# Performance work log

Hardware: AMD Instinct MI355X
Metric: run time of the kernel (lower is better)

Reference implementation:

```python
import jax, jax.numpy as jnp
import numpy as np

# dims
B, S, H = 2, 256, 1024          # batch, global seq, global hidden
BH, NH = 384, 8                  # byte_hidden, num heads
HD = BH // NH                    # head dim = 48
P = 4                            # num_global_proj (seed byte positions)
S_C = 12                         # byte decode steps (= target.shape[2])
L = 4                            # num_byte_decoder_layers
V = 258                          # byte vocab (256 bytes + pad 256 + eos 257)
T = P + S_C
EOS = 257
SCALE = 1.0 / np.sqrt(HD)


def setup_inputs() -> dict:
    key = jax.random.key(0)
    ks = jax.random.split(key, 12)
    w = lambda k, shp: jax.random.normal(k, shp, jnp.float32) * 0.02
    return {
        "x": jax.random.normal(ks[0], (B, S, H), jnp.float32),
        "target": jax.random.randint(ks[1], (B, S, S_C), 0, V),
        "Wproj": w(ks[2], (H, P * BH)),
        "attn_norm": jnp.ones((L, BH), jnp.float32),
        "Wq": w(ks[3], (L, BH, BH)),
        "Wk": w(ks[4], (L, BH, BH)),
        "Wv": w(ks[5], (L, BH, BH)),
        "Wo": w(ks[6], (L, BH, BH)),
        "ffn_norm": jnp.ones((L, BH), jnp.float32),
        "W1": w(ks[7], (L, BH, 4 * BH)),
        "W2": w(ks[8], (L, 4 * BH, BH)),
        "Wlm": w(ks[9], (BH, V)),
    }


def _rms(x, g):
    return x * jax.lax.rsqrt(jnp.mean(x * x, -1, keepdims=True) + 1e-5) * g


def _block(x, kc, vc, pos, an, Wq, Wk, Wv, Wo, fn, W1, W2, causal):
    # x: [N, Lq, BH]; kc/vc: [N, T, NH, HD] KV caches; pos: static write offset
    N, Lq, _ = x.shape
    h = _rms(x, an)
    q = (h @ Wq).reshape(N, Lq, NH, HD)
    k = (h @ Wk).reshape(N, Lq, NH, HD)
    v = (h @ Wv).reshape(N, Lq, NH, HD)
    kc = jax.lax.dynamic_update_slice(kc, k, (0, pos, 0, 0))
    vc = jax.lax.dynamic_update_slice(vc, v, (0, pos, 0, 0))
    nk = pos + Lq
    sc = jnp.einsum('nqhd,nkhd->nhqk', q, kc[:, :nk]) * SCALE
    if causal:
        mask = jnp.arange(nk)[None, :] <= (pos + jnp.arange(Lq))[:, None]
        sc = jnp.where(mask[None, None], sc, jnp.float32(-1e30))
    p = jax.nn.softmax(sc, axis=-1)
    o = jnp.einsum('nhqk,nkhd->nqhd', p, vc[:, :nk]).reshape(N, Lq, BH)
    x = x + o @ Wo
    x = x + jax.nn.gelu(_rms(x, fn) @ W1, approximate=False) @ W2
    return x, kc, vc


def _forward(x, Wproj, attn_norm, Wq, Wk, Wv, Wo, ffn_norm, W1, W2, Wlm):
    N = B * S
    x0 = (x.reshape(N, H) @ Wproj).reshape(N, P, BH)
    x_out = jnp.zeros((N, T, BH), x0.dtype).at[:, :P].set(x0)
    kc = [jnp.zeros((N, T, NH, HD), x0.dtype) for _ in range(L)]
    vc = [jnp.zeros((N, T, NH, HD), x0.dtype) for _ in range(L)]
    finished = jnp.zeros((N,), bool)
    for i in range(S_C):
        if i == 0:
            pos, xi, causal = 0, x_out[:, :P], True          # prefill seed bytes
        else:
            pos, xi, causal = P + i - 1, x_out[:, P + i - 1:P + i], False  # decode 1 token
        for l in range(L):
            xi, kc[l], vc[l] = _block(xi, kc[l], vc[l], pos,
                                      attn_norm[l], Wq[l], Wk[l], Wv[l], Wo[l],
                                      ffn_norm[l], W1[l], W2[l], causal)
        gen = xi[:, -1]                                       # [N, BH]
        unf = ~finished
        # scatter only unfinished streams back (finished stay zero, as in torch)
        x_out = x_out.at[:, P + i].set(jnp.where(unf[:, None], gen, jnp.float32(0.0)))
        finished = finished | (unf & (jnp.argmax(gen, -1) == EOS))
    return x_out.reshape(B, S, T, BH)[:, :, P:, :] @ Wlm      # [B,S,S_C,V]


def reference(x, target, Wproj, attn_norm, Wq, Wk, Wv, Wo, ffn_norm, W1, W2, Wlm):
    del target  # only sets S_c (static here)
    return _forward(x, Wproj, attn_norm, Wq, Wk, Wv, Wo, ffn_norm, W1, W2, Wlm)
```

## Files before the change

### kernel.cpp

```cpp
#include <hip/hip_runtime.h>
#include <hip/hip_bf16.h>


constexpr int H_IN  = 1024;
constexpr int BH    = 384;
constexpr int NH    = 8;
constexpr int HD    = 48;
constexpr int PP    = 4;
constexpr int S_CNT = 12;
constexpr int NL    = 4;
constexpr int NV    = 258;
constexpr int TT    = 16;
constexpr int NSEQ  = 512;
constexpr int EOS_I = 257;
constexpr int NTH   = 768;
constexpr float RSCALE = 0.14433756729740646f;

typedef _Float16 h2 __attribute__((ext_vector_type(2)));
typedef _Float16 h8 __attribute__((ext_vector_type(8)));

union W16 { h8 v8; h2 h[4]; _Float16 e[8]; };

template<int N> struct IC { static constexpr int value = N; };

__device__ __forceinline__ float fdot2(h2 a, h2 b, float c) {
#if __has_builtin(__builtin_amdgcn_fdot2)
  return __builtin_amdgcn_fdot2(a, b, c, false);
#else
  return c + (float)a.x * (float)b.x + (float)a.y * (float)b.y;
#endif
}

__global__ __launch_bounds__(256)
void pack8_kernel(const float* __restrict__ src, const float* __restrict__ g,
                  h8* __restrict__ dst, int C) {
  int c  = blockIdx.x * 256 + threadIdx.x;
  int j8 = blockIdx.y;
  if (c < C) {
    h8 v;
    #pragma unroll
    for (int r = 0; r < 8; r++) {
      int row = 8 * j8 + r;
      float s = g ? g[row] : 1.0f;
      v[r] = (_Float16)(src[(size_t)row * C + c] * s);
    }
    dst[(size_t)j8 * C + c] = v;
  }
}

__global__ __launch_bounds__(NTH)
void decoder_kernel(const float* __restrict__ x,
                    const h8* __restrict__ Wproj8,
                    const h8* __restrict__ Wq8,
                    const h8* __restrict__ Wk8,
                    const h8* __restrict__ Wv8,
                    const h8* __restrict__ Wo8,
                    const h8* __restrict__ W18,
                    const h8* __restrict__ W28,
                    const h8* __restrict__ Wlm8,
                    float* __restrict__ out,
                    _Float16* __restrict__ kbuf,
                    _Float16* __restrict__ vbuf)
{
  __shared__ float xs[2][4][BH];
  __shared__ __align__(16) _Float16 xh[2][4][BH];
  __shared__ __align__(16) _Float16 qh[2][4][BH];
  __shared__ __align__(16) _Float16 oh[2][4][BH];
  __shared__ __align__(16) _Float16 k_cur[2][4][BH];
  __shared__ __align__(16) _Float16 v_cur[2][4][BH];
  __shared__ float sc[2][NH][4][TT];
  __shared__ __align__(16) union Scr {
    float qkvp[3][2][4][BH];
    float wop[2][4][BH];
    struct { __align__(16) _Float16 f1h[2][4][4*BH];
             float w2p[2][4][BH]; } ffn;
    __align__(16) _Float16 xin[2][H_IN];
  } scr;
  __shared__ float redsq[2][4][6];
  __shared__ float redv[12];
  __shared__ int   redi[12];
  __shared__ int   fin[2];

  const int tid = threadIdx.x;
  const int kg  = tid / BH;
  const int col = tid - kg * BH;
  const int sq  = kg;
  const int wid = tid >> 6;
  const int w6  = wid % 6;
  const int seq0 = blockIdx.x * 2;

  if (tid < 2) fin[tid] = 0;

  for (int s = 0; s < 2; s++) {
    const size_t base = (size_t)(seq0 + s) * H_IN;
    for (int j = tid; j < H_IN; j += NTH) scr.xin[s][j] = (_Float16)x[base + j];
  }
  __syncthreads();
  {
    float acc[2][2] = {};
    for (int j8 = 0; j8 < H_IN / 8; j8 += 4) {
      W16 w0[4], w1[4];
      #pragma unroll
      for (int u = 0; u < 4; u++) {
        w0[u].v8 = Wproj8[(size_t)(j8 + u) * (PP * BH) + tid];
        w1[u].v8 = Wproj8[(size_t)(j8 + u) * (PP * BH) + tid + NTH];
      }
      #pragma unroll
      for (int u = 0; u < 4; u++)
        #pragma unroll
        for (int s = 0; s < 2; s++) {
          W16 hv; hv.v8 = *(const h8*)&scr.xin[s][(j8 + u) * 8];
          #pragma unroll
          for (int r = 0; r < 4; r++) {
            acc[s][0] = fdot2(hv.h[r], w0[u].h[r], acc[s][0]);
            acc[s][1] = fdot2(hv.h[r], w1[u].h[r], acc[s][1]);
          }
        }
    }
    const int m0 = tid / BH, cc = tid - m0 * BH;
    #pragma unroll
    for (int s = 0; s < 2; s++) {
      xs[s][m0][cc]     = acc[s][0];  xh[s][m0][cc]     = (_Float16)acc[s][0];
      xs[s][m0 + 2][cc] = acc[s][1];  xh[s][m0 + 2][cc] = (_Float16)acc[s][1];
      float r0 = acc[s][0] * acc[s][0], r1 = acc[s][1] * acc[s][1];
      #pragma unroll
      for (int off = 32; off; off >>= 1) {
        r0 += __shfl_down(r0, off, 64); r1 += __shfl_down(r1, off, 64);
      }
      if ((tid & 63) == 0) { redsq[s][m0][w6] = r0; redsq[s][m0 + 2][w6] = r1; }
    }
  }
  __syncthreads();

  auto layers = [&](auto ntc, int pos, bool causal) {
    constexpr int NT = decltype(ntc)::value;
    const int nk = pos + NT;
    for (int l = 0; l < NL; l++) {
      {
        const size_t wb = ((size_t)l * 48 + kg * 24) * BH + col;
        float aq[2][NT] = {}, ak[2][NT] = {}, av[2][NT] = {};
        for (int j8 = 0; j8 < 24; j8 += 4) {
          W16 wq[4], wk[4], wv[4];
          #pragma unroll
          for (int u = 0; u < 4; u++) {
            wq[u].v8 = Wq8[wb + (size_t)(j8 + u) * BH];
            wk[u].v8 = Wk8[wb + (size_t)(j8 + u) * BH];
            wv[u].v8 = Wv8[wb + (size_t)(j8 + u) * BH];
          }
          #pragma unroll
          for (int u = 0; u < 4; u++)
            #pragma unroll
            for (int s = 0; s < 2; s++)
              #pragma unroll
              for (int tok = 0; tok < NT; tok++) {
                W16 hv; hv.v8 = *(const h8*)&xh[s][tok][(kg * 24 + j8 + u) * 8];
                #pragma unroll
                for (int r = 0; r < 4; r++) {
                  aq[s][tok] = fdot2(hv.h[r], wq[u].h[r], aq[s][tok]);
                  ak[s][tok] = fdot2(hv.h[r], wk[u].h[r], ak[s][tok]);
                  av[s][tok] = fdot2(hv.h[r], wv[u].h[r], av[s][tok]);
                }
              }
        }
        {
          const int so = kg ^ 1;
          #pragma unroll
          for (int tok = 0; tok < NT; tok++) {
            scr.qkvp[0][so][tok][col] = aq[so][tok];
            scr.qkvp[1][so][tok][col] = ak[so][tok];
            scr.qkvp[2][so][tok][col] = av[so][tok];
          }
        }
        __syncthreads();
        {
          const int s = kg;
          const size_t cb = (((size_t)(seq0 + s) * NL + l) * TT + pos) * BH + col;
          #pragma unroll
          for (int tok = 0; tok < NT; tok++) {
            float ss = redsq[s][tok][0] + redsq[s][tok][1] + redsq[s][tok][2] +
                       redsq[s][tok][3] + redsq[s][tok][4] + redsq[s][tok][5];
            float sca = rsqrtf(ss * (1.0f / BH) + 1e-5f);
            float kv_ = (ak[s][tok] + scr.qkvp[1][s][tok][col]) * sca;
            float vv_ = (av[s][tok] + scr.qkvp[2][s][tok][col]) * sca;
            qh[s][tok][col] = (_Float16)((aq[s][tok] + scr.qkvp[0][s][tok][col]) * sca * RSCALE);
            k_cur[s][tok][col] = (_Float16)kv_;
            v_cur[s][tok][col] = (_Float16)vv_;
            kbuf[cb + (size_t)tok * BH] = (_Float16)kv_;
            vbuf[cb + (size_t)tok * BH] = (_Float16)vv_;
          }
        }
        __syncthreads();
      }
      if constexpr (NT == 1) {
        if (tid < 2 * NH * TT) {
          const int s = tid >> 7, r = tid & 127, h = r >> 4, j = r & 15;
          float d = -1e30f;
          if (j < nk) {
            const h8* kp8 = (j == pos)
                ? (const h8*)&k_cur[s][0][h * HD]
                : (const h8*)(kbuf + (((size_t)(seq0 + s) * NL + l) * TT + j) * BH + h * HD);
            d = 0.f;
            #pragma unroll
            for (int c6 = 0; c6 < 6; c6++) {
              W16 kk, qq;
              kk.v8 = kp8[c6];
              qq.v8 = *(const h8*)&qh[s][0][h * HD + c6 * 8];
              #pragma unroll
              for (int rr = 0; rr < 4; rr++) d = fdot2(qq.h[rr], kk.h[rr], d);
            }
          }
          float m = d;
          #pragma unroll
          for (int off = 8; off; off >>= 1) m = fmaxf(m, __shfl_xor(m, off, 16));
          float e = expf(d - m);
          float den = e;
          #pragma unroll
          for (int off = 8; off; off >>= 1) den += __shfl_xor(den, off, 16);
          sc[s][h][0][j] = e * (1.0f / den);
        }
        __syncthreads();
      } else {
        {
          const int nu = 2 * NH * NT * nk;
          if (tid < nu) {
            int s = tid / (NH * NT * nk), r = tid % (NH * NT * nk);
            int h = r / (NT * nk); int r2 = r % (NT * nk);
            int qi = r2 / nk, j = r2 % nk;
            float d;
            if (causal && j > pos + qi) d = -1e30f;
            else {
              d = 0.f;
              #pragma unroll
              for (int c6 = 0; c6 < 6; c6++) {
                W16 kk, qq;
                kk.v8 = *(const h8*)&k_cur[s][j][h * HD + c6 * 8];
                qq.v8 = *(const h8*)&qh[s][qi][h * HD + c6 * 8];
                #pragma unroll
                for (int rr = 0; rr < 4; rr++) d = fdot2(qq.h[rr], kk.h[rr], d);
              }
            }
            sc[s][h][qi][j] = d;
          }
        }
        __syncthreads();
        {
          const int nr = 2 * NH * NT;
          if (tid < nr) {
            int s = tid / (NH * NT), r = tid % (NH * NT);
            int h = r / NT, qi = r % NT;
            float m = -3.0e38f;
            for (int j = 0; j < nk; j++) m = fmaxf(m, sc[s][h][qi][j]);
            float den = 0.f;
            for (int j = 0; j < nk; j++) {
              float e = expf(sc[s][h][qi][j] - m);
              sc[s][h][qi][j] = e; den += e;
            }
            float inv = 1.0f / den;
            for (int j = 0; j < nk; j++) sc[s][h][qi][j] *= inv;
          }
        }
        __syncthreads();
      }
      {
        const size_t vb = (((size_t)(seq0 + sq) * NL + l) * TT) * BH + col;
        const int h = col / HD;
        #pragma unroll
        for (int tok = 0; tok < NT; tok++) {
          float acc = 0.f;
          if constexpr (NT == 1) {
            int j = 0;
            for (; j + 4 <= pos; j += 4) {
              float v0 = (float)vbuf[vb + (size_t)(j + 0) * BH];
              float v1 = (float)vbuf[vb + (size_t)(j + 1) * BH];
              float v2 = (float)vbuf[vb + (size_t)(j + 2) * BH];
              float v3 = (float)vbuf[vb + (size_t)(j + 3) * BH];
              acc += sc[sq][h][0][j] * v0 + sc[sq][h][0][j + 1] * v1 +
                     sc[sq][h][0][j + 2] * v2 + sc[sq][h][0][j + 3] * v3;
            }
            for (; j < pos; j++)
              acc += sc[sq][h][0][j] * (float)vbuf[vb + (size_t)j * BH];
            acc += sc[sq][h][0][pos] * (float)v_cur[sq][0][col];
          } else {
            #pragma unroll
            for (int j = 0; j < 4; j++)
              acc += sc[sq][h][tok][j] * (float)v_cur[sq][j][col];
          }
          oh[sq][tok][col] = (_Float16)acc;
        }
      }
      __syncthreads();
      {
        const size_t wb = ((size_t)l * 48 + kg * 24) * BH + col;
        float ao[2][NT] = {};
        for (int j8 = 0; j8 < 24; j8 += 8) {
          W16 w[8];
          #pragma unroll
          for (int u = 0; u < 8; u++) w[u].v8 = Wo8[wb + (size_t)(j8 + u) * BH];
          #pragma unroll
          for (int u = 0; u < 8; u++)
            #pragma unroll
            for (int s = 0; s < 2; s++)
              #pragma unroll
              for (int tok = 0; tok < NT; tok++) {
                W16 hv; hv.v8 = *(const h8*)&oh[s][tok][(kg * 24 + j8 + u) * 8];
                #pragma unroll
                for (int r = 0; r < 4; r++)
                  ao[s][tok] = fdot2(hv.h[r], w[u].h[r], ao[s][tok]);
              }
        }
        {
          const int so = kg ^ 1;
          #pragma unroll
          for (int tok = 0; tok < NT; tok++) scr.wop[so][tok][col] = ao[so][tok];
        }
        __syncthreads();
        {
          const int s = kg;
          #pragma unroll
          for (int tok = 0; tok < NT; tok++) {
            float xn = xs[s][tok][col] + ao[s][tok] + scr.wop[s][tok][col];
            xs[s][tok][col] = xn; xh[s][tok][col] = (_Float16)xn;
            float r = xn * xn;
            #pragma unroll
            for (int off = 32; off; off >>= 1) r += __shfl_down(r, off, 64);
            if ((tid & 63) == 0) redsq[s][tok][w6] = r;
          }
        }
        __syncthreads();
      }
      {
        float a1[2][NT][2] = {};
        for (int j8 = 0; j8 < 48; j8 += 4) {
          W16 w0[4], w1[4];
          #pragma unroll
          for (int u = 0; u < 4; u++) {
            w0[u].v8 = W18[((size_t)(l * 48 + j8 + u)) * (4 * BH) + tid];
            w1[u].v8 = W18[((size_t)(l * 48 + j8 + u)) * (4 * BH) + tid + NTH];
          }
          #pragma unroll
          for (int u = 0; u < 4; u++)
            #pragma unroll
            for (int s = 0; s < 2; s++)
              #pragma unroll
              for (int t = 0; t < NT; t++) {
                W16 hv; hv.v8 = *(const h8*)&xh[s][t][(j8 + u) * 8];
                #pragma unroll
                for (int r = 0; r < 4; r++) {
                  a1[s][t][0] = fdot2(hv.h[r], w0[u].h[r], a1[s][t][0]);
                  a1[s][t][1] = fdot2(hv.h[r], w1[u].h[r], a1[s][t][1]);
                }
              }
        }
        #pragma unroll
        for (int s = 0; s < 2; s++)
          #pragma unroll
          for (int t = 0; t < NT; t++) {
            float ss = redsq[s][t][0] + redsq[s][t][1] + redsq[s][t][2] +
                       redsq[s][t][3] + redsq[s][t][4] + redsq[s][t][5];
            float sca = rsqrtf(ss * (1.0f / BH) + 1e-5f);
            float z0 = a1[s][t][0] * sca, z1 = a1[s][t][1] * sca;
            scr.ffn.f1h[s][t][tid]       = (_Float16)(0.5f * z0 * (1.0f + erff(z0 * 0.7071067811865476f)));
            scr.ffn.f1h[s][t][tid + NTH] = (_Float16)(0.5f * z1 * (1.0f + erff(z1 * 0.7071067811865476f)));
          }
        __syncthreads();
        {
          float a2[2][NT] = {};
          for (int j8 = 0; j8 < 96; j8 += 8) {
            W16 w[8];
            #pragma unroll
            for (int u = 0; u < 8; u++)
              w[u].v8 = W28[((size_t)(l * 192 + kg * 96 + j8 + u)) * BH + col];
            #pragma unroll
            for (int u = 0; u < 8; u++)
              #pragma unroll
              for (int s = 0; s < 2; s++)
                #pragma unroll
                for (int t = 0; t < NT; t++) {
                  W16 fv; fv.v8 = *(const h8*)&scr.ffn.f1h[s][t][(kg * 96 + j8 + u) * 8];
                  #pragma unroll
                  for (int r = 0; r < 4; r++)
                    a2[s][t] = fdot2(fv.h[r], w[u].h[r], a2[s][t]);
                }
          }
          {
            const int so = kg ^ 1;
            #pragma unroll
            for (int t = 0; t < NT; t++) scr.ffn.w2p[so][t][col] = a2[so][t];
          }
          __syncthreads();
          {
            const int s = kg;
            #pragma unroll
            for (int t = 0; t < NT; t++) {
              float xn = xs[s][t][col] + a2[s][t] + scr.ffn.w2p[s][t][col];
              xs[s][t][col] = xn; xh[s][t][col] = (_Float16)xn;
              float r = xn * xn;
              #pragma unroll
              for (int off = 32; off; off >>= 1) r += __shfl_down(r, off, 64);
              if ((tid & 63) == 0) redsq[s][t][w6] = r;
            }
          }
          __syncthreads();
        }
      }
    }
  };

  for (int i = 0; i < S_CNT; i++) {
    int grow;
    if (i == 0) { layers(IC<4>{}, 0, true);           grow = 3; }
    else        { layers(IC<1>{}, PP + i - 1, false); grow = 0; }

    {
      float gen = xs[sq][grow][col];
      float v = gen; int idx = col;
      #pragma unroll
      for (int off = 32; off; off >>= 1) {
        float v2 = __shfl_down(v, off, 64); int i2 = __shfl_down(idx, off, 64);
        if (v2 > v || (v2 == v && i2 < idx)) { v = v2; idx = i2; }
      }
      if ((tid & 63) == 0) { redv[wid] = v; redi[wid] = idx; }
      float nxt = fin[sq] ? 0.0f : gen;
      xs[sq][0][col] = nxt; xh[sq][0][col] = (_Float16)nxt;
      float r = nxt * nxt;
      #pragma unroll
      for (int off = 32; off; off >>= 1) r += __shfl_down(r, off, 64);
      if ((tid & 63) == 0) redsq[sq][0][w6] = r;
      __syncthreads();
    }
    {
      if (col == 0) {
        const int b = sq * 6;
        float bv = redv[b]; int bi = redi[b];
        for (int w = 1; w < 6; w++)
          if (redv[b + w] > bv || (redv[b + w] == bv && redi[b + w] < bi)) {
            bv = redv[b + w]; bi = redi[b + w];
          }
        if (bi == EOS_I) fin[sq] = 1;
      }
      if (col < NV) {
        float acc = 0.f;
        for (int j8 = 0; j8 < 48; j8 += 8) {
          W16 w[8];
          #pragma unroll
          for (int u = 0; u < 8; u++) w[u].v8 = Wlm8[(size_t)(j8 + u) * NV + col];
          #pragma unroll
          for (int u = 0; u < 8; u++) {
            W16 gv; gv.v8 = *(const h8*)&xh[sq][0][(j8 + u) * 8];
            #pragma unroll
            for (int r = 0; r < 4; r++) acc = fdot2(gv.h[r], w[u].h[r], acc);
          }
        }
        out[((size_t)(seq0 + sq) * S_CNT + i) * NV + col] = acc;
      }
      __syncthreads();
    }
  }
}

extern "C" void kernel_launch(void* const* d_in, const int* in_sizes, int n_in,
                              void* d_out, int out_size, void* d_ws, size_t ws_size,
                              hipStream_t stream) {
  const float* x     = (const float*)d_in[0];
  const float* Wproj = (const float*)d_in[2];
  const float* an    = (const float*)d_in[3];
  const float* Wq    = (const float*)d_in[4];
  const float* Wk    = (const float*)d_in[5];
  const float* Wv    = (const float*)d_in[6];
  const float* Wo    = (const float*)d_in[7];
  const float* fn    = (const float*)d_in[8];
  const float* W1    = (const float*)d_in[9];
  const float* W2    = (const float*)d_in[10];
  const float* Wlm   = (const float*)d_in[11];
  float* out = (float*)d_out;
  (void)ws_size; (void)in_sizes; (void)n_in; (void)out_size;

  h8* w = (h8*)d_ws;
  const int n_proj = (H_IN / 8) * (PP * BH);
  const int n_qkvo = NL * (BH / 8) * BH;
  const int n_w1   = NL * (BH / 8) * (4 * BH);
  const int n_w2   = NL * (4 * BH / 8) * BH;
  const int n_lm   = (BH / 8) * NV;
  h8* Wproj_p = w;  w += n_proj;
  h8* Wq_p    = w;  w += n_qkvo;
  h8* Wk_p    = w;  w += n_qkvo;
  h8* Wv_p    = w;  w += n_qkvo;
  h8* Wo_p    = w;  w += n_qkvo;
  h8* W1_p    = w;  w += n_w1;
  h8* W2_p    = w;  w += n_w2;
  h8* Wlm_p   = w;  w += n_lm;
  const size_t kv_elems = (size_t)NSEQ * NL * TT * BH;
  _Float16* kbuf = (_Float16*)w;
  _Float16* vbuf = kbuf + kv_elems;

  auto pack = [&](const float* src, const float* g, h8* dst, int R, int C) {
    dim3 grid((C + 255) / 256, R / 8);
    pack8_kernel<<<grid, 256, 0, stream>>>(src, g, dst, C);
  };
  pack(Wproj, nullptr, Wproj_p, H_IN,        PP * BH);
  pack(Wq,    an,      Wq_p,    NL * BH,     BH);
  pack(Wk,    an,      Wk_p,    NL * BH,     BH);
  pack(Wv,    an,      Wv_p,    NL * BH,     BH);
  pack(Wo,    nullptr, Wo_p,    NL * BH,     BH);
  pack(W1,    fn,      W1_p,    NL * BH,     4 * BH);
  pack(W2,    nullptr, W2_p,    NL * 4 * BH, BH);
  pack(Wlm,   nullptr, Wlm_p,   BH,          NV);

  decoder_kernel<<<NSEQ / 2, NTH, 0, stream>>>(
      x, Wproj_p, Wq_p, Wk_p, Wv_p, Wo_p, W1_p, W2_p, Wlm_p, out, kbuf, vbuf);
}
```

Before: 2.334 ms.

## Stream decoder weights through per-wave LDS ring via global_load_lds

Replaces the register-batched global loads of Wq/Wk/Wv/Wo/W1/W2 with a per-wave 4-deep LDS ring fed by global_load_lds. Explicit vmcnt waits keep several rows in flight while the dot products run. The aim is to hide weight-streaming latency and reduce register pressure. In exchange, Q/K/V and W1's two halves are now separate passes that each re-read the activation vector. Each row also takes an extra LDS round trip and serialized waitcnt/sched barriers, which may cut memory-level parallelism compared with the earlier 12 concurrent loads.

```diff
diff --git a/kernel.cpp b/kernel.cpp
--- a/kernel.cpp
+++ b/kernel.cpp
@@ -29,6 +29,30 @@
 #else
   return c + (float)a.x * (float)b.x + (float)a.y * (float)b.y;
 #endif
+}
+
+__device__ __forceinline__ void gll16(const h8* g, h8* l) {
+  __builtin_amdgcn_global_load_lds(
+      (const __attribute__((address_space(1))) void*)g,
+      (__attribute__((address_space(3))) void*)l,
+      16, 0, 0);
+}
+
+template <typename A, typename F>
+__device__ __forceinline__ void stream16(int n, h8* ring_w, int lane, A addr, F consume) {
+  const int pre = n < 4 ? n : 4;
+  for (int i = 0; i < pre; ++i) gll16(addr(i) + lane, ring_w + (i & 3) * 64);
+  for (int i = 0; i < n; ++i) {
+    const int sl = i & 3;
+    if (i + 4 < n) { asm volatile("s_waitcnt vmcnt(3)" ::: "memory"); }
+    else           { asm volatile("s_waitcnt vmcnt(0)" ::: "memory"); }
+    __builtin_amdgcn_sched_barrier(0);
+    W16 wv; wv.v8 = ring_w[sl * 64 + lane];
+    asm volatile("s_waitcnt lgkmcnt(0)" ::: "memory");
+    __builtin_amdgcn_sched_barrier(0);
+    if (i + 4 < n) gll16(addr(i + 4) + lane, ring_w + sl * 64);
+    consume(i, wv);
+  }
 }
 
 __global__ __launch_bounds__(256)
@@ -68,6 +92,7 @@
   __shared__ __align__(16) _Float16 oh[2][4][BH];
   __shared__ __align__(16) _Float16 k_cur[2][4][BH];
   __shared__ __align__(16) _Float16 v_cur[2][4][BH];
+  __shared__ __align__(16) h8 ring[12][4 * 64];
   __shared__ float sc[2][NH][4][TT];
   __shared__ __align__(16) union Scr {
     float qkvp[3][2][4][BH];
@@ -87,7 +112,10 @@
   const int sq  = kg;
   const int wid = tid >> 6;
   const int w6  = wid % 6;
+  const int lane = tid & 63;
+  const int wcol0 = col - lane;
   const int seq0 = blockIdx.x * 2;
+  h8* const ring_w = &ring[wid][0];
 
   if (tid < 2) fin[tid] = 0;
 
@@ -137,31 +165,44 @@
     const int nk = pos + NT;
     for (int l = 0; l < NL; l++) {
       {
-        const size_t wb = ((size_t)l * 48 + kg * 24) * BH + col;
+        const size_t wrow0 = (size_t)l * 48 + kg * 24;
         float aq[2][NT] = {}, ak[2][NT] = {}, av[2][NT] = {};
-        for (int j8 = 0; j8 < 24; j8 += 4) {
-          W16 wq[4], wk[4], wv[4];
-          #pragma unroll
-          for (int u = 0; u < 4; u++) {
-            wq[u].v8 = Wq8[wb + (size_t)(j8 + u) * BH];
-            wk[u].v8 = Wk8[wb + (size_t)(j8 + u) * BH];
-            wv[u].v8 = Wv8[wb + (size_t)(j8 + u) * BH];
-          }
-          #pragma unroll
-          for (int u = 0; u < 4; u++)
+        stream16(24, ring_w, lane,
+          [&](int i) { return Wq8 + (wrow0 + i) * BH + wcol0; },
+          [&](int i, W16 wv) {
             #pragma unroll
             for (int s = 0; s < 2; s++)
               #pragma unroll
-              for (int tok = 0; tok < NT; tok++) {
-                W16 hv; hv.v8 = *(const h8*)&xh[s][tok][(kg * 24 + j8 + u) * 8];
-                #pragma unroll
-                for (int r = 0; r < 4; r++) {
-                  aq[s][tok] = fdot2(hv.h[r], wq[u].h[r], aq[s][tok]);
-                  ak[s][tok] = fdot2(hv.h[r], wk[u].h[r], ak[s][tok]);
-                  av[s][tok] = fdot2(hv.h[r], wv[u].h[r], av[s][tok]);
-                }
-              }
-        }
+              for (int t = 0; t < NT; t++) {
+                W16 hv; hv.v8 = *(const h8*)&xh[s][t][(kg * 24 + i) * 8];
+                #pragma unroll
+                for (int r = 0; r < 4; r++) aq[s][t] = fdot2(hv.h[r], wv.h[r], aq[s][t]);
+              }
+          });
+        stream16(24, ring_w, lane,
+          [&](int i) { return Wk8 + (wrow0 + i) * BH + wcol0; },
+          [&](int i, W16 wv) {
+            #pragma unroll
+            for (int s = 0; s < 2; s++)
+              #pragma unroll
+              for (int t = 0; t < NT; t++) {
+                W16 hv; hv.v8 = *(const h8*)&xh[s][t][(kg * 24 + i) * 8];
+                #pragma unroll
+                for (int r = 0; r < 4; r++) ak[s][t] = fdot2(hv.h[r], wv.h[r], ak[s][t]);
+              }
+          });
+        stream16(24, ring_w, lane,
+          [&](int i) { return Wv8 + (wrow0 + i) * BH + wcol0; },
+          [&](int i, W16 wv) {
+            #pragma unroll
+            for (int s = 0; s < 2; s++)
+              #pragma unroll
+              for (int t = 0; t < NT; t++) {
+                W16 hv; hv.v8 = *(const h8*)&xh[s][t][(kg * 24 + i) * 8];
+                #pragma unroll
+                for (int r = 0; r < 4; r++) av[s][t] = fdot2(hv.h[r], wv.h[r], av[s][t]);
+              }
+          });
         {
           const int so = kg ^ 1;
           #pragma unroll
@@ -290,24 +331,20 @@
       }
       __syncthreads();
       {
-        const size_t wb = ((size_t)l * 48 + kg * 24) * BH + col;
+        const size_t wrow0 = (size_t)l * 48 + kg * 24;
         float ao[2][NT] = {};
-        for (int j8 = 0; j8 < 24; j8 += 8) {
-          W16 w[8];
-          #pragma unroll
-          for (int u = 0; u < 8; u++) w[u].v8 = Wo8[wb + (size_t)(j8 + u) * BH];
-          #pragma unroll
-          for (int u = 0; u < 8; u++)
+        stream16(24, ring_w, lane,
+          [&](int i) { return Wo8 + (wrow0 + i) * BH + wcol0; },
+          [&](int i, W16 wv) {
             #pragma unroll
             for (int s = 0; s < 2; s++)
               #pragma unroll
-              for (int tok = 0; tok < NT; tok++) {
-                W16 hv; hv.v8 = *(const h8*)&oh[s][tok][(kg * 24 + j8 + u) * 8];
-                #pragma unroll
-                for (int r = 0; r < 4; r++)
-                  ao[s][tok] = fdot2(hv.h[r], w[u].h[r], ao[s][tok]);
-              }
-        }
+              for (int t = 0; t < NT; t++) {
+                W16 hv; hv.v8 = *(const h8*)&oh[s][t][(kg * 24 + i) * 8];
+                #pragma unroll
+                for (int r = 0; r < 4; r++) ao[s][t] = fdot2(hv.h[r], wv.h[r], ao[s][t]);
+              }
+          });
         {
           const int so = kg ^ 1;
           #pragma unroll
@@ -330,27 +367,31 @@
       }
       {
         float a1[2][NT][2] = {};
-        for (int j8 = 0; j8 < 48; j8 += 4) {
-          W16 w0[4], w1[4];
-          #pragma unroll
-          for (int u = 0; u < 4; u++) {
-            w0[u].v8 = W18[((size_t)(l * 48 + j8 + u)) * (4 * BH) + tid];
-            w1[u].v8 = W18[((size_t)(l * 48 + j8 + u)) * (4 * BH) + tid + NTH];
-          }
-          #pragma unroll
-          for (int u = 0; u < 4; u++)
+        const size_t w1row0 = (size_t)l * 48;
+        stream16(48, ring_w, lane,
+          [&](int i) { return W18 + (w1row0 + i) * (4 * BH) + (wid * 64); },
+          [&](int i, W16 wv) {
             #pragma unroll
             for (int s = 0; s < 2; s++)
               #pragma unroll
               for (int t = 0; t < NT; t++) {
-                W16 hv; hv.v8 = *(const h8*)&xh[s][t][(j8 + u) * 8];
-                #pragma unroll
-                for (int r = 0; r < 4; r++) {
-                  a1[s][t][0] = fdot2(hv.h[r], w0[u].h[r], a1[s][t][0]);
-                  a1[s][t][1] = fdot2(hv.h[r], w1[u].h[r], a1[s][t][1]);
-                }
-              }
-        }
+                W16 hv; hv.v8 = *(const h8*)&xh[s][t][i * 8];
+                #pragma unroll
+                for (int r = 0; r < 4; r++) a1[s][t][0] = fdot2(hv.h[r], wv.h[r], a1[s][t][0]);
+              }
+          });
+        stream16(48, ring_w, lane,
+          [&](int i) { return W18 + (w1row0 + i) * (4 * BH) + (wid * 64 + NTH); },
+          [&](int i, W16 wv) {
+            #pragma unroll
+            for (int s = 0; s < 2; s++)
+              #pragma unroll
+              for (int t = 0; t < NT; t++) {
+                W16 hv; hv.v8 = *(const h8*)&xh[s][t][i * 8];
+                #pragma unroll
+                for (int r = 0; r < 4; r++) a1[s][t][1] = fdot2(hv.h[r], wv.h[r], a1[s][t][1]);
+              }
+          });
         #pragma unroll
         for (int s = 0; s < 2; s++)
           #pragma unroll
@@ -365,23 +406,19 @@
         __syncthreads();
         {
           float a2[2][NT] = {};
-          for (int j8 = 0; j8 < 96; j8 += 8) {
-            W16 w[8];
-            #pragma unroll
-            for (int u = 0; u < 8; u++)
-              w[u].v8 = W28[((size_t)(l * 192 + kg * 96 + j8 + u)) * BH + col];
-            #pragma unroll
-            for (int u = 0; u < 8; u++)
+          const size_t w2row0 = (size_t)l * 192 + kg * 96;
+          stream16(96, ring_w, lane,
+            [&](int i) { return W28 + (w2row0 + i) * BH + wcol0; },
+            [&](int i, W16 wv) {
               #pragma unroll
               for (int s = 0; s < 2; s++)
                 #pragma unroll
                 for (int t = 0; t < NT; t++) {
-                  W16 fv; fv.v8 = *(const h8*)&scr.ffn.f1h[s][t][(kg * 96 + j8 + u) * 8];
+                  W16 fv; fv.v8 = *(const h8*)&scr.ffn.f1h[s][t][(kg * 96 + i) * 8];
                   #pragma unroll
-                  for (int r = 0; r < 4; r++)
-                    a2[s][t] = fdot2(fv.h[r], w[u].h[r], a2[s][t]);
+                  for (int r = 0; r < 4; r++) a2[s][t] = fdot2(fv.h[r], wv.h[r], a2[s][t]);
                 }
-          }
+            });
           {
             const int so = kg ^ 1;
             #pragma unroll
```

After: 4.668 ms. +100.0%, slower.
